# Kernel optimization log

Hardware: AMD Instinct MI355X
Metric: run time of the kernel (lower is better)

The kernel has to match this reference:

```python
import jax, jax.numpy as jnp
import numpy as np
import math

MUL = 32          # multiplicity of 0e and 1o node irreps
NATTR = 4         # node attribute scalars (species one-hot)
NBASIS = 10       # radial basis size
HID = 64          # radial MLP hidden width
RMAX = 4.0
NUM_NEIGHBORS = 32.0
NLAYERS = 2
OUT_DIM = 16
NGRAPH = 8
SQRT3 = math.sqrt(3.0)


def smooth_cutoff(xr):
    u = 2.0 * (xr - 1.0)
    y = (1.0 - jnp.cos(math.pi * u)) * 0.5
    return jnp.where(u > 0.0, 0.0, jnp.where(u < -1.0, 1.0, y))


def fctp(s, v, attr, W0, W1, fan_in):
    # FullyConnectedTensorProduct with scalar attrs: mixes channels u x a -> w.
    norm = 1.0 / math.sqrt(fan_in)
    so = jnp.einsum('nu,na,uaw->nw', s, attr, W0) * norm
    vo = jnp.einsum('nui,na,uaw->nwi', v, attr, W1) * norm
    return so, vo


def setup_inputs() -> dict:
    key = jax.random.key(0)
    ks = jax.random.split(key, 16)
    N, E = 10000, 320000
    x = jax.random.normal(ks[0], (N, MUL * 4), dtype=jnp.float32)  # 32x0e + 32x1o
    node_attr = jax.random.uniform(ks[1], (N, NATTR), dtype=jnp.float32)
    edge_vec = jax.random.normal(ks[2], (E, 3), dtype=jnp.float32)
    edge_src = jax.random.randint(ks[3], (E,), 0, N, dtype=jnp.int32)
    edge_dst = jax.random.randint(ks[4], (E,), 0, N, dtype=jnp.int32)
    batch = jnp.sort(jax.random.randint(ks[5], (N,), 0, NGRAPH, dtype=jnp.int32))
    g = lambda k, shp: jax.random.normal(k, shp, dtype=jnp.float32)
    L = NLAYERS
    return {
        'x': x, 'node_attr': node_attr, 'edge_vec': edge_vec, 'batch': batch,
        'edge_src': edge_src, 'edge_dst': edge_dst,
        'Wsc0': g(ks[6], (L, MUL, NATTR, MUL)),
        'Wsc1': g(ks[7], (L, MUL, NATTR, MUL)),
        'Wl10': g(ks[8], (L, MUL, NATTR, MUL)),
        'Wl11': g(ks[9], (L, MUL, NATTR, MUL)),
        'Wfc1': g(ks[10], (L, NBASIS, HID)),
        'Wfc2': g(ks[11], (L, HID, 4 * MUL)),
        'Wl20': g(ks[12], (L, 2 * MUL, NATTR, MUL)),
        'Wl21': g(ks[13], (L, 2 * MUL, NATTR, MUL)),
        'Wread': g(ks[14], (MUL, NATTR, OUT_DIM)),
    }


def reference(x, node_attr, edge_vec, batch, edge_src, edge_dst,
              Wsc0, Wsc1, Wl10, Wl11, Wfc1, Wfc2, Wl20, Wl21, Wread):
    N = x.shape[0]
    s = x[:, :MUL]                                # [N, 32]  scalars (0e)
    v = x[:, MUL:].reshape(N, MUL, 3)             # [N, 32, 3] vectors (1o)

    # edge geometry -> spherical harmonics (component norm) + radial embedding
    length = jnp.linalg.norm(edge_vec, axis=-1)               # [E]
    unit = edge_vec / (length + 1e-9)[:, None]
    Y1 = SQRT3 * unit                                         # l=1 SH, Y0 == 1
    centers = jnp.linspace(0.0, RMAX, NBASIS)
    emb = jnp.exp(-(((length[:, None] - centers) / (RMAX / NBASIS)) ** 2))
    emb = emb * smooth_cutoff(length / RMAX)[:, None]         # [E, 10]

    c_s, c_x = math.sin(math.pi / 8), math.cos(math.pi / 8)

    for l in range(NLAYERS):
        # self connection and first linear (FCTP with node attrs)
        sc_s, sc_v = fctp(s, v, node_attr, Wsc0[l], Wsc1[l], MUL * NATTR)
        xs, xv = fctp(s, v, node_attr, Wl10[l], Wl11[l], MUL * NATTR)

        # radial MLP -> per-edge 'uvu' tensor-product weights (4 paths x MUL)
        h = jax.nn.silu(emb @ Wfc1[l] / math.sqrt(NBASIS))
        w = (h @ Wfc2[l]) / math.sqrt(HID)
        w = w.reshape(-1, 4, MUL)                             # [E, 4, 32]

        sE = xs[edge_src]                                     # [E, 32]
        vE = xv[edge_src]                                     # [E, 32, 3]
        # CG paths kept by Convolution (out in irreps_out or 0e):
        mid0a = w[:, 0] * sE                                   # 0e x 0e -> 0e
        mid0b = w[:, 1] * jnp.einsum('ei,eui->eu', Y1, vE) / SQRT3  # 1o x 1o -> 0e
        mid1a = w[:, 2][:, :, None] * sE[:, :, None] * Y1[:, None, :]  # 0e x 1o -> 1o
        mid1b = w[:, 3][:, :, None] * vE                       # 1o x 0e -> 1o
        mid_s = jnp.concatenate([mid0a, mid0b], axis=1)        # [E, 64]
        mid_v = jnp.concatenate([mid1a, mid1b], axis=1)        # [E, 64, 3]

        inv = 1.0 / math.sqrt(NUM_NEIGHBORS)
        agg_s = jax.ops.segment_sum(mid_s, edge_dst, num_segments=N) * inv
        agg_v = jax.ops.segment_sum(mid_v, edge_dst, num_segments=N) * inv

        os_, ov = fctp(agg_s, agg_v, node_attr, Wl20[l], Wl21[l], 2 * MUL * NATTR)
        s_new = c_s * sc_s + c_x * os_
        v_new = c_s * sc_v + c_x * ov

        # gate nonlinearity (equivariant) + residual (CustomCompose)
        s = s + jax.nn.silu(s_new)
        v = v + v_new * jax.nn.sigmoid(s_new)[:, :, None]

    # scalar readout + per-graph pooling
    out_node = jnp.einsum('nu,na,uaw->nw', s, node_attr, Wread) / math.sqrt(MUL * NATTR)
    pooled = jax.ops.segment_sum(out_node, batch, num_segments=NGRAPH)
    pooled = pooled / math.sqrt(N / NGRAPH)
    return pooled
```

## Files before the change

### kernel.cpp

```cpp
#include <hip/hip_runtime.h>
#include <math.h>

#define MUL 32
#define NATTR 4
#define NBASIS 10
#define HID 64
#define OUT_DIM 16
#define NGRAPH 8
#define NT 513

#define PI_F 3.14159265358979323846f
#define SQRT3_F 1.7320508075688772f
#define INV_SQRT3_F 0.5773502691896258f
#define INV_SQRT10_F 0.31622776601683794f
#define INV_SQRTNN_F 0.17677669529663687f
#define NORM128_F 0.08838834764831845f
#define NORM256_F 0.0625f
#define C_S_F 0.3826834323650898f
#define C_X_F 0.9238795325112867f
#define CSTEP_F (4.0f/9.0f)

__device__ inline unsigned short f2bf(float x) {
    unsigned u = __float_as_uint(x);
    u += 0x7FFF + ((u >> 16) & 1);
    return (unsigned short)(u >> 16);
}
__device__ inline float bf2f(unsigned short h) {
    return __uint_as_float(((unsigned)h) << 16);
}

__device__ __forceinline__ void init_sv_body(
    int blk, const float* __restrict__ x,
    float* __restrict__ s, float* __restrict__ v, int N) {
    int i = blk * 256 + threadIdx.x;
    if (i >= N * 128) return;
    int n = i >> 7, c = i & 127;
    float val = x[i];
    if (c < 32) s[n * 32 + c] = val;
    else        v[n * 96 + (c - 32)] = val;
}

__device__ __forceinline__ void setup_weights_body(
    int blk,
    const float* __restrict__ Wsc0, const float* __restrict__ Wl10,
    const float* __restrict__ Wsc1, const float* __restrict__ Wl11,
    const float* __restrict__ Wl20, const float* __restrict__ Wl21,
    float* __restrict__ Wfp, unsigned* __restrict__ Wupk) {
    int i = blk * 256 + threadIdx.x;
    if (i < 32768) {
        int idx = i >> 12;
        int r = i & 4095;
        int l = idx >> 2, m = idx & 3;
        const float* base = (m == 0 ? Wsc0 : m == 1 ? Wl10 : m == 2 ? Wsc1 : Wl11)
                            + l * 4096;
        int u = r >> 7, rr = r & 127, a = rr >> 5, ww = rr & 31;
        Wfp[idx * 4096 + u * 128 + ww * 4 + a] = base[r];
    } else if (i < 49152) {
        int j = i - 32768;
        int l = j >> 13;
        int r = j & 8191;
        int u = r >> 7, rr = r & 127, a = rr >> 5, ww = rr & 31;
        unsigned lo = f2bf(Wl20[l * 8192 + r]);
        unsigned hi = f2bf(Wl21[l * 8192 + r]);
        Wupk[l * 8192 + u * 128 + ww * 4 + a] = lo | (hi << 16);
    }
}

__device__ __forceinline__ void tab_gen_body(
    int blk, const float* __restrict__ Wfc1, const float* __restrict__ Wfc2,
    unsigned* __restrict__ tab, float (*sh_h)[64]) {
    int g = threadIdx.x >> 6;
    int n = threadIdx.x & 63;
    int row = blk * 4 + g;
    bool valid = row < 2 * NT;
    int l = valid ? row / NT : 0;
    int i = valid ? row % NT : 0;
    float len = (float)i * (1.0f / 128.0f);
    float uu = len * 0.5f - 2.0f;
    float cut = (uu > 0.0f) ? 0.0f
              : ((uu < -1.0f) ? 1.0f : 0.5f * (1.0f - __cosf(PI_F * uu)));
    const float* W1 = Wfc1 + l * 640;
    float a = 0.f;
#pragma unroll
    for (int k = 0; k < 10; k++) {
        float d = (len - k * CSTEP_F) * 2.5f;
        float e = __expf(-d * d) * cut;
        a += e * W1[k * 64 + n];
    }
    a *= INV_SQRT10_F;
    sh_h[g][n] = a / (1.0f + __expf(-a));
    __syncthreads();
    if (!valid) return;
    const float* W2 = Wfc2 + l * 8192;
    float w0 = 0.f, w1 = 0.f;
#pragma unroll 8
    for (int nn = 0; nn < 64; nn++) {
        float hn = sh_h[g][nn];
        w0 += hn * W2[nn * 128 + n];
        w1 += hn * W2[nn * 128 + 64 + n];
    }
    w0 *= 0.125f; w1 *= 0.125f;
    tab[(size_t)l * NT * 64 + i * 64 + n] =
        (unsigned)f2bf(w0) | ((unsigned)f2bf(w1) << 16);
}

__device__ __forceinline__ void csr_count_body(
    int blk, const int* __restrict__ edst, int* __restrict__ cnt, int E) {
    int e = blk * 256 + threadIdx.x;
    if (e < E) atomicAdd(&cnt[edst[e]], 1);
}

__device__ __forceinline__ void csr_fill_body(
    int blk, const int* __restrict__ edst, const int* __restrict__ esrc,
    const float* __restrict__ edge_vec, int* __restrict__ cursor,
    float* __restrict__ vec_csr, int E) {
    int e = blk * 256 + threadIdx.x;
    if (e < E) {
        int d = edst[e];
        int p = atomicAdd(&cursor[d], 1);
        float4 vv = {edge_vec[e * 3 + 0], edge_vec[e * 3 + 1], edge_vec[e * 3 + 2],
                     __int_as_float(esrc[e])};
        *(float4*)(vec_csr + (size_t)p * 4) = vv;
    }
}

__device__ __forceinline__ void node_fctp_body(
    int blk, int path,
    const float* __restrict__ s, const float* __restrict__ v,
    const float* __restrict__ attr, const float* __restrict__ Wfp,
    float* __restrict__ sc_s, float* __restrict__ sc_v,
    float* __restrict__ xsv, int N, char* smem) {
    float* w0 = (float*)smem;
    float* w1 = (float*)(smem + 16384);
    float (*sh)[96] = (float(*)[96])(smem + 32768);
    int ln = threadIdx.x >> 5, w = threadIdx.x & 31;
    const float4* W0p = (const float4*)(Wfp + path * 8192);
    const float4* W1p = (const float4*)(Wfp + path * 8192 + 4096);
    for (int i = threadIdx.x; i < 1024; i += 256) {
        ((float4*)w0)[i] = W0p[i];
        ((float4*)w1)[i] = W1p[i];
    }
    for (int g = 0; g < 2; g++) {
        int n = blk * 16 + g * 8 + ln;
        bool valid = n < N;
        __syncthreads();
        if (valid) {
            if (path == 0) {
                sh[ln][w] = s[n * 32 + w];
            } else {
                sh[ln][w * 3 + 0] = v[n * 96 + w * 3 + 0];
                sh[ln][w * 3 + 1] = v[n * 96 + w * 3 + 1];
                sh[ln][w * 3 + 2] = v[n * 96 + w * 3 + 2];
            }
        }
        __syncthreads();
        if (!valid) continue;
        float4 at = *(const float4*)(attr + n * 4);
        if (path == 0) {
            float acc0 = 0.f, acc1 = 0.f;
            for (int u = 0; u < 32; u++) {
                float su = sh[ln][u];
                float4 W0v = *(const float4*)(w0 + u * 128 + w * 4);
                float4 W1v = *(const float4*)(w1 + u * 128 + w * 4);
                float d0 = at.x * W0v.x + at.y * W0v.y + at.z * W0v.z + at.w * W0v.w;
                float d1 = at.x * W1v.x + at.y * W1v.y + at.z * W1v.z + at.w * W1v.w;
                acc0 += su * d0;
                acc1 += su * d1;
            }
            sc_s[n * 32 + w] = acc0 * NORM128_F;
            xsv[(size_t)n * 128 + w * 4 + 3] = acc1 * NORM128_F;
        } else {
            float a00 = 0, a01 = 0, a02 = 0, a10 = 0, a11 = 0, a12 = 0;
            for (int u = 0; u < 32; u++) {
                float vu0 = sh[ln][u * 3 + 0];
                float vu1 = sh[ln][u * 3 + 1];
                float vu2 = sh[ln][u * 3 + 2];
                float4 W0v = *(const float4*)(w0 + u * 128 + w * 4);
                float4 W1v = *(const float4*)(w1 + u * 128 + w * 4);
                float d0 = at.x * W0v.x + at.y * W0v.y + at.z * W0v.z + at.w * W0v.w;
                float d1 = at.x * W1v.x + at.y * W1v.y + at.z * W1v.z + at.w * W1v.w;
                a00 += vu0 * d0; a01 += vu1 * d0; a02 += vu2 * d0;
                a10 += vu0 * d1; a11 += vu1 * d1; a12 += vu2 * d1;
            }
            sc_v[n * 96 + w * 3 + 0] = a00 * NORM128_F;
            sc_v[n * 96 + w * 3 + 1] = a01 * NORM128_F;
            sc_v[n * 96 + w * 3 + 2] = a02 * NORM128_F;
            float* xp = xsv + (size_t)n * 128 + w * 4;
            xp[0] = a10 * NORM128_F;
            xp[1] = a11 * NORM128_F;
            xp[2] = a12 * NORM128_F;
        }
    }
}

__global__ __launch_bounds__(256) void mega1(
    int nTab, int nInit, int nSetup,
    const float* __restrict__ x, float* __restrict__ s, float* __restrict__ v,
    const float* __restrict__ Wfc1, const float* __restrict__ Wfc2,
    const float* __restrict__ Wsc0, const float* __restrict__ Wl10,
    const float* __restrict__ Wsc1, const float* __restrict__ Wl11,
    const float* __restrict__ Wl20, const float* __restrict__ Wl21,
    float* __restrict__ Wfp, unsigned* __restrict__ Wupk,
    unsigned* __restrict__ tab,
    const int* __restrict__ edst, int* __restrict__ cnt, int N, int E) {
    __shared__ float sh_h[4][64];
    int b = blockIdx.x;
    if (b < nTab) { tab_gen_body(b, Wfc1, Wfc2, tab, sh_h); return; }
    b -= nTab;
    if (b < nInit) { init_sv_body(b, x, s, v, N); return; }
    b -= nInit;
    if (b < nSetup) {
        setup_weights_body(b, Wsc0, Wl10, Wsc1, Wl11, Wl20, Wl21, Wfp, Wupk);
        return;
    }
    b -= nSetup;
    csr_count_body(b, edst, cnt, E);
}

__global__ void csr_scan(const int* __restrict__ cnt, int* __restrict__ off,
                         int* __restrict__ cursor, int N) {
    __shared__ int sums[256];
    int t = threadIdx.x;
    int chunk = (N + 255) / 256;
    int lo = t * chunk, hi = lo + chunk; if (hi > N) hi = N;
    int s = 0;
    for (int i = lo; i < hi; i++) s += cnt[i];
    sums[t] = s;
    __syncthreads();
    for (int d = 1; d < 256; d <<= 1) {
        int v = (t >= d) ? sums[t - d] : 0;
        __syncthreads();
        sums[t] += v;
        __syncthreads();
    }
    int run = (t == 0) ? 0 : sums[t - 1];
    for (int i = lo; i < hi; i++) {
        off[i] = run; cursor[i] = run;
        run += cnt[i];
    }
}

__global__ __launch_bounds__(256, 4) void mega2(
    int nFill, int nF,
    const int* __restrict__ edst, const int* __restrict__ esrc,
    const float* __restrict__ edge_vec, int* __restrict__ cursor,
    float* __restrict__ vec_csr, int E,
    const float* __restrict__ s, const float* __restrict__ v,
    const float* __restrict__ attr, const float* __restrict__ Wfp,
    float* __restrict__ sc_s, float* __restrict__ sc_v,
    float* __restrict__ xsv, int N) {
    __shared__ __align__(16) char smem[35840];
    int b = blockIdx.x;
    if (b < nFill) {
        csr_fill_body(b, edst, esrc, edge_vec, cursor, vec_csr, E);
        return;
    }
    b -= nFill;
    node_fctp_body(b % nF, b / nF, s, v, attr, Wfp, sc_s, sc_v, xsv, N, smem);
}

__global__ __launch_bounds__(256, 4) void fctp_only(
    int nF,
    const float* __restrict__ s, const float* __restrict__ v,
    const float* __restrict__ attr, const float* __restrict__ Wfp,
    float* __restrict__ sc_s, float* __restrict__ sc_v,
    float* __restrict__ xsv, int N) {
    __shared__ __align__(16) char smem[35840];
    node_fctp_body(blockIdx.x % nF, blockIdx.x / nF, s, v, attr, Wfp,
                   sc_s, sc_v, xsv, N, smem);
}

__global__ __launch_bounds__(256, 4) void gather_update(
    const int* __restrict__ off, const int* __restrict__ cnt,
    const unsigned* __restrict__ tab,
    const float* __restrict__ vec_csr, const float* __restrict__ xsv,
    const float* __restrict__ attr, const unsigned* __restrict__ Wupk,
    const float* __restrict__ sc_s, const float* __restrict__ sc_v,
    float* __restrict__ s, float* __restrict__ v, int N) {
    __shared__ float red[2][8][32];
    __shared__ float part[2][4][32];
    int pair = threadIdx.x >> 7;
    int node = blockIdx.x * 2 + pair;
    int ql = threadIdx.x & 127;
    int quarter = ql >> 5;
    int u = ql & 31;
    bool active = node < N;
    int o = 0, deg = 0;
    if (active) { o = off[node]; deg = cnt[node]; }
    float as0 = 0, as1 = 0;
    float av00 = 0, av01 = 0, av02 = 0, av10 = 0, av11 = 0, av12 = 0;

    auto body = [&](int slot) {
        size_t p = (size_t)slot;
        float4 vv = *(const float4*)(vec_csr + p * 4);
        int src = __float_as_int(vv.w);
        float len = sqrtf(vv.x * vv.x + vv.y * vv.y + vv.z * vv.z);
        float rinv = SQRT3_F / (len + 1e-9f);
        float y0 = vv.x * rinv, y1 = vv.y * rinv, y2 = vv.z * rinv;
        float t = fminf(len, 3.99995f) * 128.0f;
        int ti = (int)t;
        float fr = t - (float)ti;
        const unsigned* tr = tab + ti * 64 + u;
        unsigned qa0 = tr[0],  qa1 = tr[32];
        unsigned qb0 = tr[64], qb1 = tr[96];
        float4 x4 = *(const float4*)(xsv + (size_t)src * 128 + u * 4);
        float wa0 = bf2f((unsigned short)qa0), wb0 = bf2f((unsigned short)qb0);
        float wc0 = bf2f((unsigned short)(qa0 >> 16)), wd0 = bf2f((unsigned short)(qb0 >> 16));
        float wa1 = bf2f((unsigned short)qa1), wb1 = bf2f((unsigned short)qb1);
        float wc1 = bf2f((unsigned short)(qa1 >> 16)), wd1 = bf2f((unsigned short)(qb1 >> 16));
        float wa = wa0 + fr * (wb0 - wa0);
        float wc = wc0 + fr * (wd0 - wc0);
        float wb = wa1 + fr * (wb1 - wa1);
        float wd = wc1 + fr * (wd1 - wc1);
        as0 += wa * x4.w;
        as1 += wb * (y0 * x4.x + y1 * x4.y + y2 * x4.z) * INV_SQRT3_F;
        float tt = wc * x4.w;
        av00 += tt * y0;  av01 += tt * y1;  av02 += tt * y2;
        av10 += wd * x4.x; av11 += wd * x4.y; av12 += wd * x4.z;
    };

    int i = quarter;
    for (; i + 4 < deg; i += 8) { body(o + i); body(o + i + 4); }
    for (; i < deg; i += 4) body(o + i);

    as0 += __shfl_down(as0, 32);  as1 += __shfl_down(as1, 32);
    av00 += __shfl_down(av00, 32); av01 += __shfl_down(av01, 32); av02 += __shfl_down(av02, 32);
    av10 += __shfl_down(av10, 32); av11 += __shfl_down(av11, 32); av12 += __shfl_down(av12, 32);

    int lane = threadIdx.x & 63;
    int upper_wave = (threadIdx.x >> 6) & 1;
    if (upper_wave && lane < 32) {
        red[pair][0][u] = as0;  red[pair][1][u] = as1;
        red[pair][2][u] = av00; red[pair][3][u] = av01; red[pair][4][u] = av02;
        red[pair][5][u] = av10; red[pair][6][u] = av11; red[pair][7][u] = av12;
    }
    __syncthreads();
    if (!upper_wave && lane < 32) {
        red[pair][0][u] = (as0 + red[pair][0][u]) * INV_SQRTNN_F;
        red[pair][1][u] = (as1 + red[pair][1][u]) * INV_SQRTNN_F;
        red[pair][2][u] = (av00 + red[pair][2][u]) * INV_SQRTNN_F;
        red[pair][3][u] = (av01 + red[pair][3][u]) * INV_SQRTNN_F;
        red[pair][4][u] = (av02 + red[pair][4][u]) * INV_SQRTNN_F;
        red[pair][5][u] = (av10 + red[pair][5][u]) * INV_SQRTNN_F;
        red[pair][6][u] = (av11 + red[pair][6][u]) * INV_SQRTNN_F;
        red[pair][7][u] = (av12 + red[pair][7][u]) * INV_SQRTNN_F;
    }
    __syncthreads();

    {
        int half = quarter >> 1;
        int ub = (quarter & 1) * 16;
        int w = u;
        float4 at = {0.f, 0.f, 0.f, 0.f};
        if (active) at = *(const float4*)(attr + node * 4);
        const float* rs = red[pair][half];
        const float* r0 = red[pair][2 + 3 * half];
        const float* r1 = red[pair][3 + 3 * half];
        const float* r2 = red[pair][4 + 3 * half];
        float pacc = 0.f, pa0 = 0.f, pa1 = 0.f, pa2 = 0.f;
#pragma unroll
        for (int k = 0; k < 16; k++) {
            int j = ub + k;
            float gs = rs[j], g0 = r0[j], g1 = r1[j], g2 = r2[j];
            uint4 pv = *(const uint4*)(Wupk + (half * 32 + j) * 128 + w * 4);
            float w20x = bf2f((unsigned short)pv.x), w21x = bf2f((unsigned short)(pv.x >> 16));
            float w20y = bf2f((unsigned short)pv.y), w21y = bf2f((unsigned short)(pv.y >> 16));
            float w20z = bf2f((unsigned short)pv.z), w21z = bf2f((unsigned short)(pv.z >> 16));
            float w20w = bf2f((unsigned short)pv.w), w21w = bf2f((unsigned short)(pv.w >> 16));
            float d0 = at.x * w20x + at.y * w20y + at.z * w20z + at.w * w20w;
            float d1 = at.x * w21x + at.y * w21y + at.z * w21z + at.w * w21w;
            pacc += gs * d0;
            pa0 += g0 * d1; pa1 += g1 * d1; pa2 += g2 * d1;
        }
        pacc += __shfl_down(pacc, 32);
        pa0 += __shfl_down(pa0, 32);
        pa1 += __shfl_down(pa1, 32);
        pa2 += __shfl_down(pa2, 32);
        if (upper_wave && lane < 32) {
            part[pair][0][u] = pacc;
            part[pair][1][u] = pa0;
            part[pair][2][u] = pa1;
            part[pair][3][u] = pa2;
        }
        __syncthreads();
        if (active && !upper_wave && lane < 32) {
            pacc += part[pair][0][u];
            pa0 += part[pair][1][u];
            pa1 += part[pair][2][u];
            pa2 += part[pair][3][u];
            float os = pacc * NORM256_F;
            float sn = C_S_F * sc_s[node * 32 + w] + C_X_F * os;
            float sig = 1.0f / (1.0f + __expf(-sn));
            s[node * 32 + w] += sn * sig;
            float ov0 = pa0 * NORM256_F, ov1 = pa1 * NORM256_F, ov2 = pa2 * NORM256_F;
            v[node * 96 + w * 3 + 0] += (C_S_F * sc_v[node * 96 + w * 3 + 0] + C_X_F * ov0) * sig;
            v[node * 96 + w * 3 + 1] += (C_S_F * sc_v[node * 96 + w * 3 + 1] + C_X_F * ov1) * sig;
            v[node * 96 + w * 3 + 2] += (C_S_F * sc_v[node * 96 + w * 3 + 2] + C_X_F * ov2) * sig;
        }
    }
}

__global__ __launch_bounds__(256) void readout(
    const float* __restrict__ s, const float* __restrict__ attr,
    const float* __restrict__ Wread, const int* __restrict__ batch,
    float* __restrict__ out, int N, float pool_scale) {
    __shared__ float wr[2048];
    __shared__ float red[NGRAPH * 16];
    for (int i = threadIdx.x; i < 2048; i += 256) wr[i] = Wread[i];
    if (threadIdx.x < NGRAPH * 16) red[threadIdx.x] = 0.f;
    __syncthreads();
    int ln = threadIdx.x >> 4, w = threadIdx.x & 15;
    for (int g = 0; g < 4; g++) {
        int n = blockIdx.x * 64 + g * 16 + ln;
        if (n < N) {
            float4 at = *(const float4*)(attr + n * 4);
            float fa[4] = {at.x, at.y, at.z, at.w};
            float acc = 0.f;
            for (int u = 0; u < 32; u++) {
                float su = s[n * 32 + u];
                int base = u * 64 + w;
#pragma unroll
                for (int a = 0; a < 4; a++) acc += su * fa[a] * wr[base + a * 16];
            }
            atomicAdd(&red[batch[n] * 16 + w], acc);
        }
    }
    __syncthreads();
    if (threadIdx.x < NGRAPH * 16) {
        float val = red[threadIdx.x];
        if (val != 0.f)
            atomicAdd(&out[threadIdx.x], val * NORM128_F * pool_scale);
    }
}

extern "C" void kernel_launch(void* const* d_in, const int* in_sizes, int n_in,
                              void* d_out, int out_size, void* d_ws, size_t ws_size,
                              hipStream_t stream) {
    const float* x        = (const float*)d_in[0];
    const float* nattr    = (const float*)d_in[1];
    const float* edge_vec = (const float*)d_in[2];
    const int*   batch    = (const int*)d_in[3];
    const int*   esrc     = (const int*)d_in[4];
    const int*   edst     = (const int*)d_in[5];
    const float* Wsc0  = (const float*)d_in[6];
    const float* Wsc1  = (const float*)d_in[7];
    const float* Wl10  = (const float*)d_in[8];
    const float* Wl11  = (const float*)d_in[9];
    const float* Wfc1  = (const float*)d_in[10];
    const float* Wfc2  = (const float*)d_in[11];
    const float* Wl20  = (const float*)d_in[12];
    const float* Wl21  = (const float*)d_in[13];
    const float* Wread = (const float*)d_in[14];

    int N = in_sizes[0] / (MUL * 4);
    int E = in_sizes[2] / 3;

    float* p = (float*)d_ws;
    float* vec_csr = p; p += (size_t)E * 4;
    unsigned* tab = (unsigned*)p; p += 2 * NT * 64;
    float* Wfp    = p; p += 32768;
    unsigned* Wupk = (unsigned*)p; p += 16384;
    float* s_buf  = p; p += (size_t)N * 32;
    float* v_buf  = p; p += (size_t)N * 96;
    float* sc_s   = p; p += (size_t)N * 32;
    float* sc_v   = p; p += (size_t)N * 96;
    float* xsv    = p; p += (size_t)N * 128;
    int* cnt     = (int*)p; p += N;
    int* off     = (int*)p; p += N;
    int* cursor  = (int*)p; p += N;

    hipMemsetAsync(d_out, 0, (size_t)out_size * sizeof(float), stream);
    hipMemsetAsync(cnt, 0, (size_t)N * sizeof(int), stream);

    int nTab   = (2 * NT + 3) / 4;
    int nInit  = (N * 128 + 255) / 256;
    int nSetup = 192;
    int nCount = (E + 255) / 256;
    mega1<<<nTab + nInit + nSetup + nCount, 256, 0, stream>>>(
        nTab, nInit, nSetup, x, s_buf, v_buf,
        Wfc1, Wfc2, Wsc0, Wl10, Wsc1, Wl11, Wl20, Wl21,
        Wfp, Wupk, tab, edst, cnt, N, E);

    csr_scan<<<1, 256, 0, stream>>>(cnt, off, cursor, N);

    int nFill = (E + 255) / 256;
    int nF = (N + 15) / 16;
    mega2<<<nFill + 2 * nF, 256, 0, stream>>>(
        nFill, nF, edst, esrc, edge_vec, cursor, vec_csr, E,
        s_buf, v_buf, nattr, Wfp, sc_s, sc_v, xsv, N);

    int nG = (N + 1) / 2;

    gather_update<<<nG, 256, 0, stream>>>(
        off, cnt, tab, vec_csr, xsv, nattr, Wupk,
        sc_s, sc_v, s_buf, v_buf, N);
    fctp_only<<<2 * nF, 256, 0, stream>>>(
        nF, s_buf, v_buf, nattr, Wfp + 16384, sc_s, sc_v, xsv, N);

    gather_update<<<nG, 256, 0, stream>>>(
        off, cnt, tab + NT * 64, vec_csr, xsv, nattr, Wupk + 8192,
        sc_s, sc_v, s_buf, v_buf, N);

    float pool_scale = (float)(1.0 / sqrt((double)N / (double)NGRAPH));
    readout<<<(N + 63) / 64, 256, 0, stream>>>(
        s_buf, nattr, Wread, batch, (float*)d_out, N, pool_scale);
}
```

Measured before the change: 289.3 us.

## Precompute per-edge spherical/table indices and pack radial table as base+delta uint4

During CSR fill, each edge's normalized direction, table index and fraction are computed once and stored, so the two gather passes no longer recompute sqrt and division per edge per lane. The radial weight table is repacked into one uint4 per (bin, channel) holding the base values and bf16 deltas, so each lookup is a single 16-byte load instead of four scattered 4-byte loads. The cost is an extra per-edge uint2 array read in every gather, a small conversion pass, and extra rounding from storing the deltas in bf16.

```diff
diff --git a/kernel.cpp b/kernel.cpp
--- a/kernel.cpp
+++ b/kernel.cpp
@@ -104,6 +104,28 @@
         (unsigned)f2bf(w0) | ((unsigned)f2bf(w1) << 16);
 }
 
+__device__ __forceinline__ void tab4_body(
+    int blk, const unsigned* __restrict__ tab, unsigned* __restrict__ tab4) {
+    int id = blk * 256 + threadIdx.x;
+    if (id >= 2 * 512 * 32) return;
+    int l = id >> 14;
+    int r = id & 16383;
+    int ti = r >> 5, u = r & 31;
+    const unsigned* tb = tab + (size_t)l * NT * 64 + ti * 64;
+    unsigned a0 = tb[u],      a1 = tb[u + 32];
+    unsigned b0 = tb[64 + u], b1 = tb[64 + u + 32];
+    float d0l = bf2f((unsigned short)b0) - bf2f((unsigned short)a0);
+    float d0h = bf2f((unsigned short)(b0 >> 16)) - bf2f((unsigned short)(a0 >> 16));
+    float d1l = bf2f((unsigned short)b1) - bf2f((unsigned short)a1);
+    float d1h = bf2f((unsigned short)(b1 >> 16)) - bf2f((unsigned short)(a1 >> 16));
+    uint4 q;
+    q.x = a0;
+    q.y = a1;
+    q.z = (unsigned)f2bf(d0l) | ((unsigned)f2bf(d0h) << 16);
+    q.w = (unsigned)f2bf(d1l) | ((unsigned)f2bf(d1h) << 16);
+    ((uint4*)tab4)[((size_t)l * 512 + ti) * 32 + u] = q;
+}
+
 __device__ __forceinline__ void csr_count_body(
     int blk, const int* __restrict__ edst, int* __restrict__ cnt, int E) {
     int e = blk * 256 + threadIdx.x;
@@ -113,14 +135,21 @@
 __device__ __forceinline__ void csr_fill_body(
     int blk, const int* __restrict__ edst, const int* __restrict__ esrc,
     const float* __restrict__ edge_vec, int* __restrict__ cursor,
-    float* __restrict__ vec_csr, int E) {
+    float* __restrict__ vec_csr, unsigned* __restrict__ tifr, int E) {
     int e = blk * 256 + threadIdx.x;
     if (e < E) {
         int d = edst[e];
         int p = atomicAdd(&cursor[d], 1);
-        float4 vv = {edge_vec[e * 3 + 0], edge_vec[e * 3 + 1], edge_vec[e * 3 + 2],
-                     __int_as_float(esrc[e])};
+        float ex = edge_vec[e * 3 + 0], ey = edge_vec[e * 3 + 1], ez = edge_vec[e * 3 + 2];
+        float len = sqrtf(ex * ex + ey * ey + ez * ez);
+        float rinv = SQRT3_F / (len + 1e-9f);
+        float t = fminf(len, 3.99995f) * 128.0f;
+        int ti = (int)t;
+        float fr = t - (float)ti;
+        float4 vv = {ex * rinv, ey * rinv, ez * rinv, __int_as_float(esrc[e])};
         *(float4*)(vec_csr + (size_t)p * 4) = vv;
+        uint2 tf = {(unsigned)ti, __float_as_uint(fr)};
+        *(uint2*)(tifr + (size_t)p * 2) = tf;
     }
 }
 
@@ -244,19 +273,25 @@
     int nFill, int nF,
     const int* __restrict__ edst, const int* __restrict__ esrc,
     const float* __restrict__ edge_vec, int* __restrict__ cursor,
-    float* __restrict__ vec_csr, int E,
+    float* __restrict__ vec_csr, unsigned* __restrict__ tifr, int E,
     const float* __restrict__ s, const float* __restrict__ v,
     const float* __restrict__ attr, const float* __restrict__ Wfp,
     float* __restrict__ sc_s, float* __restrict__ sc_v,
-    float* __restrict__ xsv, int N) {
+    float* __restrict__ xsv, int N,
+    const unsigned* __restrict__ tab, unsigned* __restrict__ tab4) {
     __shared__ __align__(16) char smem[35840];
     int b = blockIdx.x;
     if (b < nFill) {
-        csr_fill_body(b, edst, esrc, edge_vec, cursor, vec_csr, E);
+        csr_fill_body(b, edst, esrc, edge_vec, cursor, vec_csr, tifr, E);
         return;
     }
     b -= nFill;
-    node_fctp_body(b % nF, b / nF, s, v, attr, Wfp, sc_s, sc_v, xsv, N, smem);
+    if (b < 2 * nF) {
+        node_fctp_body(b % nF, b / nF, s, v, attr, Wfp, sc_s, sc_v, xsv, N, smem);
+        return;
+    }
+    b -= 2 * nF;
+    tab4_body(b, tab, tab4);
 }
 
 __global__ __launch_bounds__(256, 4) void fctp_only(
@@ -272,8 +307,9 @@
 
 __global__ __launch_bounds__(256, 4) void gather_update(
     const int* __restrict__ off, const int* __restrict__ cnt,
-    const unsigned* __restrict__ tab,
-    const float* __restrict__ vec_csr, const float* __restrict__ xsv,
+    const unsigned* __restrict__ tab4,
+    const float* __restrict__ vec_csr, const unsigned* __restrict__ tifr,
+    const float* __restrict__ xsv,
     const float* __restrict__ attr, const unsigned* __restrict__ Wupk,
     const float* __restrict__ sc_s, const float* __restrict__ sc_v,
     float* __restrict__ s, float* __restrict__ v, int N) {
@@ -294,28 +330,19 @@
         size_t p = (size_t)slot;
         float4 vv = *(const float4*)(vec_csr + p * 4);
         int src = __float_as_int(vv.w);
-        float len = sqrtf(vv.x * vv.x + vv.y * vv.y + vv.z * vv.z);
-        float rinv = SQRT3_F / (len + 1e-9f);
-        float y0 = vv.x * rinv, y1 = vv.y * rinv, y2 = vv.z * rinv;
-        float t = fminf(len, 3.99995f) * 128.0f;
-        int ti = (int)t;
-        float fr = t - (float)ti;
-        const unsigned* tr = tab + ti * 64 + u;
-        unsigned qa0 = tr[0],  qa1 = tr[32];
-        unsigned qb0 = tr[64], qb1 = tr[96];
+        uint2 tf = *(const uint2*)(tifr + p * 2);
+        int ti = (int)tf.x;
+        float fr = __uint_as_float(tf.y);
+        uint4 tq = ((const uint4*)tab4)[((size_t)ti << 5) + u];
         float4 x4 = *(const float4*)(xsv + (size_t)src * 128 + u * 4);
-        float wa0 = bf2f((unsigned short)qa0), wb0 = bf2f((unsigned short)qb0);
-        float wc0 = bf2f((unsigned short)(qa0 >> 16)), wd0 = bf2f((unsigned short)(qb0 >> 16));
-        float wa1 = bf2f((unsigned short)qa1), wb1 = bf2f((unsigned short)qb1);
-        float wc1 = bf2f((unsigned short)(qa1 >> 16)), wd1 = bf2f((unsigned short)(qb1 >> 16));
-        float wa = wa0 + fr * (wb0 - wa0);
-        float wc = wc0 + fr * (wd0 - wc0);
-        float wb = wa1 + fr * (wb1 - wa1);
-        float wd = wc1 + fr * (wd1 - wc1);
+        float wa = bf2f((unsigned short)tq.x) + fr * bf2f((unsigned short)tq.z);
+        float wc = bf2f((unsigned short)(tq.x >> 16)) + fr * bf2f((unsigned short)(tq.z >> 16));
+        float wb = bf2f((unsigned short)tq.y) + fr * bf2f((unsigned short)tq.w);
+        float wd = bf2f((unsigned short)(tq.y >> 16)) + fr * bf2f((unsigned short)(tq.w >> 16));
         as0 += wa * x4.w;
-        as1 += wb * (y0 * x4.x + y1 * x4.y + y2 * x4.z) * INV_SQRT3_F;
+        as1 += wb * (vv.x * x4.x + vv.y * x4.y + vv.z * x4.z) * INV_SQRT3_F;
         float tt = wc * x4.w;
-        av00 += tt * y0;  av01 += tt * y1;  av02 += tt * y2;
+        av00 += tt * vv.x;  av01 += tt * vv.y;  av02 += tt * vv.z;
         av10 += wd * x4.x; av11 += wd * x4.y; av12 += wd * x4.z;
     };
 
@@ -457,7 +484,9 @@
 
     float* p = (float*)d_ws;
     float* vec_csr = p; p += (size_t)E * 4;
+    unsigned* tifr = (unsigned*)p; p += ((size_t)E * 2 + 3) & ~(size_t)3;
     unsigned* tab = (unsigned*)p; p += 2 * NT * 64;
+    unsigned* tab4 = (unsigned*)p; p += 2 * 512 * 32 * 4;
     float* Wfp    = p; p += 32768;
     unsigned* Wupk = (unsigned*)p; p += 16384;
     float* s_buf  = p; p += (size_t)N * 32;
@@ -485,20 +514,21 @@
 
     int nFill = (E + 255) / 256;
     int nF = (N + 15) / 16;
-    mega2<<<nFill + 2 * nF, 256, 0, stream>>>(
-        nFill, nF, edst, esrc, edge_vec, cursor, vec_csr, E,
-        s_buf, v_buf, nattr, Wfp, sc_s, sc_v, xsv, N);
+    int nConv = (2 * 512 * 32 + 255) / 256;
+    mega2<<<nFill + 2 * nF + nConv, 256, 0, stream>>>(
+        nFill, nF, edst, esrc, edge_vec, cursor, vec_csr, tifr, E,
+        s_buf, v_buf, nattr, Wfp, sc_s, sc_v, xsv, N, tab, tab4);
 
     int nG = (N + 1) / 2;
 
     gather_update<<<nG, 256, 0, stream>>>(
-        off, cnt, tab, vec_csr, xsv, nattr, Wupk,
+        off, cnt, tab4, vec_csr, tifr, xsv, nattr, Wupk,
         sc_s, sc_v, s_buf, v_buf, N);
     fctp_only<<<2 * nF, 256, 0, stream>>>(
         nF, s_buf, v_buf, nattr, Wfp + 16384, sc_s, sc_v, xsv, N);
 
     gather_update<<<nG, 256, 0, stream>>>(
-        off, cnt, tab + NT * 64, vec_csr, xsv, nattr, Wupk + 8192,
+        off, cnt, tab4 + 512 * 32 * 4, vec_csr, tifr, xsv, nattr, Wupk + 8192,
         sc_s, sc_v, s_buf, v_buf, N);
 
     float pool_scale = (float)(1.0 / sqrt((double)N / (double)NGRAPH));
```

Result: faster. 276.4 us (-4.5%).
